# Optimization experiments

Measured on AMD Instinct MI355X. Metric: run time of the kernel, lower is better.

## Reference

```python
import jax, jax.numpy as jnp
import numpy as np
import math

S, HID = 2048, 2048
NH, Q_LORA, KV_LORA = 16, 1536, 512
NOPE, ROPE, VDIM = 128, 64, 128
HEAD = NOPE + ROPE  # 192
BLK = 128
EPS = 1e-6
MSCALE = 0.1 * 1.0 * math.log(40.0) + 1.0
SOFTMAX_SCALE = HEAD ** -0.5 * MSCALE * MSCALE


def _dequant(w, s, blk=BLK):
    # w: [out,in] stored quantized values, s: [ceil(out/blk), ceil(in/blk)] block scale_inv
    so = jnp.repeat(s, blk, axis=0)[: w.shape[0]]
    se = jnp.repeat(so, blk, axis=1)[:, : w.shape[1]]
    return w * se


def _mm_dq(x, w, s):
    # mm_w8a16_dq_forward: x @ dequant(w).T
    return x @ _dequant(w, s).T


def _rmsnorm(x, w, eps=EPS):
    var = jnp.mean(x * x, axis=-1, keepdims=True)
    return x * jax.lax.rsqrt(var + eps) * w


def _rotate_half(x):
    h = x.shape[-1] // 2
    return jnp.concatenate([-x[..., h:], x[..., :h]], axis=-1)


def setup_inputs() -> dict:
    key = jax.random.key(0)
    ks = jax.random.split(key, 16)
    d = {
        'hidden_states': jax.random.normal(ks[0], (S, HID), jnp.float32),
        'wq_a': jax.random.normal(ks[1], (Q_LORA, HID), jnp.float32),
        'sq_a': jax.random.uniform(ks[2], (12, 16), jnp.float32) * 0.02 + 0.005,
        'wq_b': jax.random.normal(ks[3], (NH * HEAD, Q_LORA), jnp.float32),
        'sq_b': jax.random.uniform(ks[4], (24, 12), jnp.float32) * 0.02 + 0.005,
        'wkv_a': jax.random.normal(ks[5], (KV_LORA + ROPE, HID), jnp.float32),
        'skv_a': jax.random.uniform(ks[6], (5, 16), jnp.float32) * 0.02 + 0.005,
        'wkv_b': jax.random.normal(ks[7], (NH * (NOPE + VDIM), KV_LORA), jnp.float32),
        'skv_b': jax.random.uniform(ks[8], (32, 4), jnp.float32) * 0.02 + 0.005,
        'wo': jax.random.normal(ks[9], (HID, NH * VDIM), jnp.float32),
        'so': jax.random.uniform(ks[10], (16, 16), jnp.float32) * 0.02 + 0.005,
        'q_ln_w': jnp.ones((Q_LORA,), jnp.float32),
        'kv_ln_w': jnp.ones((KV_LORA,), jnp.float32),
    }
    pos = jnp.arange(S, dtype=jnp.float32)[:, None]
    inv = 1.0 / (10000.0 ** (jnp.arange(0, ROPE, 2, dtype=jnp.float32) / ROPE))
    ang = pos * inv[None, :]
    ang = jnp.concatenate([ang, ang], axis=-1)  # [S, 64]
    d['cos'] = jnp.cos(ang)
    d['sin'] = jnp.sin(ang)
    return d


def reference(hidden_states, cos, sin, wq_a, sq_a, wq_b, sq_b, wkv_a, skv_a,
              wkv_b, skv_b, wo, so, q_ln_w, kv_ln_w):
    # Q low-rank path: q_a -> rmsnorm -> q_b
    lq = _mm_dq(hidden_states, wq_a, sq_a)                 # [S, q_lora]
    q = _mm_dq(_rmsnorm(lq, q_ln_w), wq_b, sq_b)           # [S, NH*HEAD]
    q = q.reshape(S, NH, HEAD)
    q_nope, q_pe = q[..., :NOPE], q[..., NOPE:]            # [S,NH,128], [S,NH,64]

    # KV low-rank + MQA rope path
    lkv = _mm_dq(hidden_states, wkv_a, skv_a)              # [S, kv_lora+rope]
    kv_nope = _rmsnorm(lkv[:, :KV_LORA], kv_ln_w)          # [S, kv_lora]
    k_pe = lkv[:, KV_LORA:]                                # [S, 64] (shared across heads)
    kvb = _mm_dq(kv_nope, wkv_b, skv_b).reshape(S, NH, NOPE + VDIM)
    k_nope, v = kvb[..., :NOPE], kvb[..., NOPE:]           # [S,NH,128] each

    # RoPE (rotate-half) on the pe parts
    q_pe = q_pe * cos[:, None, :] + _rotate_half(q_pe) * sin[:, None, :]
    k_pe = k_pe * cos + _rotate_half(k_pe) * sin           # [S, 64]

    # prefill MLA attention with causal mask
    scores = (jnp.einsum('shd,thd->hst', q_nope, k_nope)
              + jnp.einsum('shd,td->hst', q_pe, k_pe)) * SOFTMAX_SCALE
    causal = jnp.tril(jnp.ones((S, S), bool))
    scores = jnp.where(causal[None], scores, -jnp.inf)
    probs = jax.nn.softmax(scores, axis=-1)                # [NH,S,S]
    attn = jnp.einsum('hst,thd->shd', probs, v).reshape(S, NH * VDIM)

    return _mm_dq(attn, wo, so)                            # [S, HID]
```

## Files before the change

kernel.cpp:

```cpp
#include <hip/hip_runtime.h>

typedef unsigned short u16;
typedef unsigned int u32;
typedef __attribute__((ext_vector_type(8))) short bf16x8;
typedef __attribute__((ext_vector_type(4))) float f32x4;
typedef __attribute__((ext_vector_type(16))) float f32x16;
typedef __attribute__((ext_vector_type(4))) unsigned short u16x4;

#define S_LEN 2048
#define HIDDEN 2048
#define NHEAD 16
#define QLORA 1536
#define KVLORA 512
#define NOPE_D 128
#define ROPE_D 64
#define V_D 128
#define HEAD_D 192
#define NCOMB 2176
#define LOG2E 1.442695041f

__device__ __constant__ float SM_SCALE_C = (float)(0.07216878364870323 *
    ((0.1 * 3.6888794541139363 + 1.0) * (0.1 * 3.6888794541139363 + 1.0)));

__device__ inline u16 f2bf(float f) {
    union { float f; unsigned int u; } v; v.f = f;
    unsigned int r = v.u + 0x7FFFu + ((v.u >> 16) & 1u);
    return (u16)(r >> 16);
}
__device__ inline float bf2f(u16 b) {
    union { unsigned int u; float f; } v; v.u = ((unsigned int)b) << 16;
    return v.f;
}
__device__ inline void gload_lds16(const u16* g, u16* l) {
    __builtin_amdgcn_global_load_lds(
        (const __attribute__((address_space(1))) void*)g,
        (__attribute__((address_space(3))) void*)l, 16, 0, 0);
}

__global__ __launch_bounds__(64)
void prep_weights(const float* __restrict__ hs,
                  const float* __restrict__ wq_a, const float* __restrict__ sq_a,
                  const float* __restrict__ wq_b, const float* __restrict__ sq_b,
                  const float* __restrict__ wkv_a, const float* __restrict__ skv_a,
                  const float* __restrict__ wkv_b, const float* __restrict__ skv_b,
                  const float* __restrict__ wo, const float* __restrict__ so,
                  u16* __restrict__ hs_bf, u16* __restrict__ wcomb,
                  u16* __restrict__ wqb_bf, u16* __restrict__ wkvb_bf,
                  u16* __restrict__ wo_bf) {
    int r = blockIdx.x;
    const float* W; const float* Sc; u16* out; int K, sc_cols, n;
    if (r < 2048)                      { n = r;                     W = hs;    Sc = 0;     out = hs_bf;   K = 2048; sc_cols = 0; }
    else if (r < 2048 + 1536)          { n = r - 2048;              W = wq_a;  Sc = sq_a;  out = wcomb;   K = 2048; sc_cols = 16; }
    else if (r < 2048 + 1536 + 576)    { n = r - (2048 + 1536);     W = wkv_a; Sc = skv_a; out = wcomb + (size_t)QLORA * 2048; K = 2048; sc_cols = 16; }
    else if (r < 2048 + 1536 + 576 + 3072) { n = r - (2048 + 1536 + 576); W = wq_b; Sc = sq_b; out = wqb_bf; K = 1536; sc_cols = 12; }
    else if (r < 2048 + 1536 + 576 + 3072 + 4096) { n = r - (2048 + 1536 + 576 + 3072); W = wkv_b; Sc = skv_b; out = wkvb_bf; K = 512; sc_cols = 4; }
    else                               { n = r - (2048 + 1536 + 576 + 3072 + 4096); W = wo; Sc = so; out = wo_bf; K = 2048; sc_cols = 16; }
    for (int k = threadIdx.x * 8; k < K; k += 512) {
        float sc = Sc ? Sc[(n >> 7) * sc_cols + (k >> 7)] : 1.0f;
        f32x4 v0 = *(const f32x4*)(W + (size_t)n * K + k);
        f32x4 v1 = *(const f32x4*)(W + (size_t)n * K + k + 4);
        bf16x8 o;
        #pragma unroll
        for (int i = 0; i < 4; ++i) {
            o[i]     = (short)f2bf(v0[i] * sc);
            o[i + 4] = (short)f2bf(v1[i] * sc);
        }
        *(bf16x8*)(out + (size_t)n * K + k) = o;
    }
}

__global__ __launch_bounds__(256)
void gemm_bf16(const u16* __restrict__ A, const u16* __restrict__ W,
               void* __restrict__ C, int M, int N, int Ktot, int Ksub, int mode) {
    __shared__ u16 As[128 * 64];
    __shared__ u16 Ws[128 * 64];
    const int tid = threadIdx.x;
    const int lane = tid & 63;
    const int wv = tid >> 6;
    const int wm = wv >> 1, wn = wv & 1;
    const int gx = gridDim.x, gy = gridDim.y;
    const int nwg = gx * gy * gridDim.z;
    const int orig = blockIdx.x + gx * (blockIdx.y + gy * blockIdx.z);
    const int qq = nwg >> 3, rr = nwg & 7, xcd = orig & 7, loc = orig >> 3;
    const int wg = (xcd < rr) ? (xcd * (qq + 1) + loc)
                              : (rr * (qq + 1) + (xcd - rr) * qq + loc);
    const int bn = (wg % gx) * 128;
    const int bm = ((wg / gx) % gy) * 128;
    const int bz = wg / (gx * gy);
    const int lr = lane & 15, lk = lane >> 4;
    const int srow = lane >> 3;
    const int schunk = lane & 7;

    f32x4 acc[4][4] = {};

    const int kbeg = bz * Ksub;
    const int kend = kbeg + Ksub;
    for (int k0 = kbeg; k0 < kend; k0 += 64) {
        __syncthreads();
        #pragma unroll
        for (int i = 0; i < 4; ++i) {
            int t = (wv * 4 + i) * 8 + srow;
            int cs = (schunk ^ (t & 7)) << 3;
            gload_lds16(A + (size_t)(bm + t) * Ktot + k0 + cs, &As[(wv * 4 + i) * 512]);
            gload_lds16(W + (size_t)(bn + t) * Ktot + k0 + cs, &Ws[(wv * 4 + i) * 512]);
        }
        __syncthreads();
        #pragma unroll
        for (int kh = 0; kh < 2; ++kh) {
            bf16x8 af[4], bfr[4];
            #pragma unroll
            for (int mi = 0; mi < 4; ++mi) {
                int r = wm * 64 + mi * 16 + lr;
                af[mi] = *(const bf16x8*)&As[r * 64 + (((kh * 4 + lk) ^ (lr & 7)) << 3)];
            }
            #pragma unroll
            for (int ni = 0; ni < 4; ++ni) {
                int r = wn * 64 + ni * 16 + lr;
                bfr[ni] = *(const bf16x8*)&Ws[r * 64 + (((kh * 4 + lk) ^ (lr & 7)) << 3)];
            }
            #pragma unroll
            for (int mi = 0; mi < 4; ++mi)
                #pragma unroll
                for (int ni = 0; ni < 4; ++ni)
                    acc[mi][ni] = __builtin_amdgcn_mfma_f32_16x16x32_bf16(af[mi], bfr[ni], acc[mi][ni], 0, 0, 0);
        }
    }

    float* Pf = (mode == 2) ? ((float*)C + (size_t)bz * M * N) : (float*)C;
    #pragma unroll
    for (int mi = 0; mi < 4; ++mi)
        #pragma unroll
        for (int ni = 0; ni < 4; ++ni)
            #pragma unroll
            for (int j = 0; j < 4; ++j) {
                int r = bm + wm * 64 + mi * 16 + lk * 4 + j;
                int c = bn + wn * 64 + ni * 16 + lr;
                if (c < N) {
                    if (mode == 1) ((u16*)C)[(size_t)r * N + c] = f2bf(acc[mi][ni][j]);
                    else           Pf[(size_t)r * N + c] = acc[mi][ni][j];
                }
            }
}

__global__ __launch_bounds__(256)
void reduce_rms_comb(const float* __restrict__ P,
                     const float* __restrict__ q_ln, const float* __restrict__ kv_ln,
                     u16* __restrict__ lqn, u16* __restrict__ kvn, u16* __restrict__ kpe) {
    __shared__ float vbuf[NCOMB];
    __shared__ float r2[2][4];
    const int row = blockIdx.x;
    const float* p0 = P + (size_t)row * NCOMB;
    const float* p1 = p0 + (size_t)S_LEN * NCOMB;
    float ssq = 0.f, ssk = 0.f;
    for (int c = threadIdx.x * 4; c < NCOMB; c += 1024) {
        f32x4 a = *(const f32x4*)(p0 + c);
        f32x4 b = *(const f32x4*)(p1 + c);
        f32x4 v = a + b;
        *(f32x4*)&vbuf[c] = v;
        float s = v[0] * v[0] + v[1] * v[1] + v[2] * v[2] + v[3] * v[3];
        if (c < QLORA) ssq += s;
        else if (c < QLORA + KVLORA) ssk += s;
    }
    #pragma unroll
    for (int off = 1; off < 64; off <<= 1) {
        ssq += __shfl_xor(ssq, off, 64);
        ssk += __shfl_xor(ssk, off, 64);
    }
    if ((threadIdx.x & 63) == 0) {
        r2[0][threadIdx.x >> 6] = ssq;
        r2[1][threadIdx.x >> 6] = ssk;
    }
    __syncthreads();
    float rsq = rsqrtf((r2[0][0] + r2[0][1] + r2[0][2] + r2[0][3]) / (float)QLORA + 1e-6f);
    float rsk = rsqrtf((r2[1][0] + r2[1][1] + r2[1][2] + r2[1][3]) / (float)KVLORA + 1e-6f);
    for (int c = threadIdx.x * 4; c < NCOMB; c += 1024) {
        f32x4 v = *(const f32x4*)&vbuf[c];
        u16x4 o;
        if (c < QLORA) {
            #pragma unroll
            for (int j = 0; j < 4; ++j) o[j] = f2bf(v[j] * rsq * q_ln[c + j]);
            *(u16x4*)(lqn + (size_t)row * QLORA + c) = o;
        } else if (c < QLORA + KVLORA) {
            int cc = c - QLORA;
            #pragma unroll
            for (int j = 0; j < 4; ++j) o[j] = f2bf(v[j] * rsk * kv_ln[cc + j]);
            *(u16x4*)(kvn + (size_t)row * KVLORA + cc) = o;
        } else if (c < QLORA + KVLORA + ROPE_D) {
            int cc = c - QLORA - KVLORA;
            #pragma unroll
            for (int j = 0; j < 4; ++j) o[j] = f2bf(v[j]);
            *(u16x4*)(kpe + (size_t)row * ROPE_D + cc) = o;
        }
    }
}

__global__ __launch_bounds__(256)
void prep_q_frag_red(const float* __restrict__ P, const float* __restrict__ cosb,
                     const float* __restrict__ sinb, u16* __restrict__ qfrag) {
    const int sblk = blockIdx.x, h = blockIdx.y;
    const float sm = SM_SCALE_C;
    #pragma unroll
    for (int c = 0; c < 3; ++c) {
        int idx = c * 256 + threadIdx.x;
        int kk = idx >> 6;
        int lane = idx & 63;
        int s = sblk * 32 + (lane & 31);
        int d0 = kk * 16 + (lane >> 5) * 8;
        const float* p0 = P + (size_t)s * (NHEAD * HEAD_D) + h * HEAD_D;
        const float* p1 = p0 + (size_t)S_LEN * (NHEAD * HEAD_D);
        bf16x8 o;
        if (d0 < NOPE_D) {
            f32x4 a0 = *(const f32x4*)(p0 + d0), a1 = *(const f32x4*)(p0 + d0 + 4);
            f32x4 b0 = *(const f32x4*)(p1 + d0), b1 = *(const f32x4*)(p1 + d0 + 4);
            #pragma unroll
            for (int j = 0; j < 4; ++j) {
                o[j]     = (short)f2bf((a0[j] + b0[j]) * sm);
                o[j + 4] = (short)f2bf((a1[j] + b1[j]) * sm);
            }
        } else {
            int r0 = d0 - NOPE_D;
            int rp = (r0 + 32) & 63;
            float x[8], rv[8];
            {
                f32x4 a0 = *(const f32x4*)(p0 + d0), a1 = *(const f32x4*)(p0 + d0 + 4);
                f32x4 b0 = *(const f32x4*)(p1 + d0), b1 = *(const f32x4*)(p1 + d0 + 4);
                #pragma unroll
                for (int j = 0; j < 4; ++j) { x[j] = a0[j] + b0[j]; x[j + 4] = a1[j] + b1[j]; }
            }
            {
                f32x4 a0 = *(const f32x4*)(p0 + NOPE_D + rp), a1 = *(const f32x4*)(p0 + NOPE_D + rp + 4);
                f32x4 b0 = *(const f32x4*)(p1 + NOPE_D + rp), b1 = *(const f32x4*)(p1 + NOPE_D + rp + 4);
                #pragma unroll
                for (int j = 0; j < 4; ++j) { rv[j] = a0[j] + b0[j]; rv[j + 4] = a1[j] + b1[j]; }
            }
            float sign = (r0 < 32) ? -1.f : 1.f;
            #pragma unroll
            for (int j = 0; j < 8; ++j) {
                float cs = cosb[s * ROPE_D + r0 + j];
                float sn = sinb[s * ROPE_D + r0 + j];
                o[j] = (short)f2bf((x[j] * cs + sign * rv[j] * sn) * sm);
            }
        }
        *(bf16x8*)(qfrag + (((size_t)h * 64 + sblk) * 12 + kk) * 512 + lane * 8) = o;
    }
}

__global__ void reduce_out(const float* __restrict__ P, float* __restrict__ out, int n) {
    int i = (blockIdx.x * blockDim.x + threadIdx.x) * 4;
    if (i >= n) return;
    f32x4 a = *(const f32x4*)(P + i);
    f32x4 b = *(const f32x4*)(P + (size_t)n + i);
    *(f32x4*)(out + i) = a + b;
}

__global__ __launch_bounds__(256)
void prep_kv_frag(const u16* __restrict__ kvb, const u16* __restrict__ kpe,
                  const float* __restrict__ cosb, const float* __restrict__ sinb,
                  u16* __restrict__ kfrag, u16* __restrict__ vfrag) {
    __shared__ u16 Vs[32][136];
    const int sblk = blockIdx.x, h = blockIdx.y;
    #pragma unroll
    for (int it = 0; it < 2; ++it) {
        int idx = it * 256 + threadIdx.x;
        int r = idx >> 4;
        int c8 = (idx & 15) * 8;
        int s = sblk * 32 + r;
        *(bf16x8*)&Vs[r][c8] = *(const bf16x8*)(kvb + (size_t)s * (NHEAD * 256) + h * 256 + NOPE_D + c8);
    }
    #pragma unroll
    for (int c = 0; c < 3; ++c) {
        int idx = c * 256 + threadIdx.x;
        int kk = idx >> 6;
        int lane = idx & 63;
        int s = sblk * 32 + (lane & 31);
        int d0 = kk * 16 + (lane >> 5) * 8;
        bf16x8 o;
        if (d0 < NOPE_D) {
            o = *(const bf16x8*)(kvb + (size_t)s * (NHEAD * 256) + h * 256 + d0);
        } else {
            int r0 = d0 - NOPE_D;
            const u16* kp = kpe + (size_t)s * ROPE_D;
            bf16x8 x = *(const bf16x8*)(kp + r0);
            bf16x8 rv = *(const bf16x8*)(kp + ((r0 + 32) & 63));
            float sign = (r0 < 32) ? -1.f : 1.f;
            #pragma unroll
            for (int j = 0; j < 8; ++j) {
                float cs = cosb[s * ROPE_D + r0 + j];
                float sn = sinb[s * ROPE_D + r0 + j];
                o[j] = (short)f2bf(bf2f((u16)x[j]) * cs + sign * bf2f((u16)rv[j]) * sn);
            }
        }
        *(bf16x8*)(kfrag + (((size_t)h * 64 + sblk) * 12 + kk) * 512 + lane * 8) = o;
    }
    __syncthreads();
    #pragma unroll
    for (int it = 0; it < 2; ++it) {
        int idx = it * 256 + threadIdx.x;
        int fi = idx >> 6;
        int lane = idx & 63;
        int bb = fi >> 1, h16 = fi & 1;
        int col = bb * 32 + (lane & 31);
        int row0 = h16 * 16 + (lane >> 5) * 8;
        bf16x8 o;
        #pragma unroll
        for (int j = 0; j < 8; ++j) o[j] = (short)Vs[row0 + j][col];
        *(bf16x8*)(vfrag + (((size_t)h * 64 + sblk) * 8 + fi) * 512 + lane * 8) = o;
    }
}

__global__ __launch_bounds__(256, 2)
void flash_attn4(const u16* __restrict__ qfrag, const u16* __restrict__ kfrag,
                 const u16* __restrict__ vfrag, u16* __restrict__ attn) {
    __shared__ float OB[3][128][32];
    __shared__ float MB[3][2][32];

    const int tid = threadIdx.x, lane = tid & 63, wq = tid >> 6;
    const int b = blockIdx.x;
    const int t = 63 - (b >> 4);
    const int h = ((b & 7) << 1) | ((b >> 3) & 1);
    const int q0 = t * 32;
    const int lq = lane & 31;
    const int hi = lane >> 5;

    const int n = t + 1;
    const int s_lo = (wq * n) >> 2;
    const int s_hi = ((wq + 1) * n) >> 2;

    bf16x8 qfr[12];
    {
        const u16* qb = qfrag + (((size_t)h * 64 + t) * 12) * 512 + lane * 8;
        #pragma unroll
        for (int kk = 0; kk < 12; ++kk) qfr[kk] = *(const bf16x8*)(qb + kk * 512);
    }

    const u16* kfb = kfrag + ((size_t)h * 64 * 12) * 512 + lane * 8;
    const u16* vfb = vfrag + ((size_t)h * 64 * 8) * 512 + lane * 8;

    f32x16 oa[4] = {};
    float mrun = -3.0e38f, lrun = 0.f;

    bf16x8 kcur[12];
    {
        int psub = (s_lo < s_hi) ? s_lo : 0;
        const u16* kp = kfb + (size_t)psub * 12 * 512;
        #pragma unroll
        for (int kk = 0; kk < 12; ++kk)
            kcur[kk] = *(const bf16x8*)(kp + kk * 512);
    }

    for (int sub = s_lo; sub < s_hi; ++sub) {
        f32x16 s0 = {}, s1 = {};
        __builtin_amdgcn_s_setprio(1);
        #pragma unroll
        for (int kk = 0; kk < 12; kk += 2) {
            s0 = __builtin_amdgcn_mfma_f32_32x32x16_bf16(kcur[kk], qfr[kk], s0, 0, 0, 0);
            s1 = __builtin_amdgcn_mfma_f32_32x32x16_bf16(kcur[kk + 1], qfr[kk + 1], s1, 0, 0, 0);
        }
        __builtin_amdgcn_s_setprio(0);
        {
            int nsub = (sub + 1 < s_hi) ? sub + 1 : sub;
            const u16* kp = kfb + (size_t)nsub * 12 * 512;
            #pragma unroll
            for (int kk = 0; kk < 12; ++kk)
                kcur[kk] = *(const bf16x8*)(kp + kk * 512);
        }
        bf16x8 va[8];
        {
            const u16* vp = vfb + (size_t)sub * 8 * 512;
            #pragma unroll
            for (int fi = 0; fi < 8; ++fi)
                va[fi] = *(const bf16x8*)(vp + fi * 512);
        }
        f32x16 sv = s0 + s1;
        if (sub == t) {
            #pragma unroll
            for (int r = 0; r < 16; ++r) {
                int krow = (r & 3) + 8 * (r >> 2) + 4 * hi;
                if (krow > lq) sv[r] = -3.0e38f;
            }
        }
        float tm = sv[0];
        #pragma unroll
        for (int r = 1; r < 16; ++r) tm = fmaxf(tm, sv[r]);
        tm = fmaxf(tm, __shfl_xor(tm, 32, 64));
        if (!__all(tm - mrun <= 8.f)) {
            float mn = fmaxf(mrun, tm);
            float scl = exp2f((mrun - mn) * LOG2E);
            mrun = mn;
            lrun *= scl;
            #pragma unroll
            for (int bb = 0; bb < 4; ++bb)
                #pragma unroll
                for (int r = 0; r < 16; ++r) oa[bb][r] *= scl;
        }
        float p[16];
        float psum = 0.f;
        #pragma unroll
        for (int r = 0; r < 16; ++r) {
            p[r] = exp2f((sv[r] - mrun) * LOG2E);
            psum += p[r];
        }
        psum += __shfl_xor(psum, 32, 64);
        lrun += psum;
        u32 pw[8], sw[8];
        #pragma unroll
        for (int i = 0; i < 8; ++i)
            pw[i] = (u32)f2bf(p[2 * i]) | ((u32)f2bf(p[2 * i + 1]) << 16);
        #pragma unroll
        for (int i = 0; i < 8; ++i)
            sw[i] = (u32)__shfl_xor((int)pw[i], 32, 64);
        union { u32 w[4]; bf16x8 v; } bf0, bf1;
        bf0.w[0] = hi ? sw[2] : pw[0];
        bf0.w[1] = hi ? sw[3] : pw[1];
        bf0.w[2] = hi ? pw[2] : sw[0];
        bf0.w[3] = hi ? pw[3] : sw[1];
        bf1.w[0] = hi ? sw[6] : pw[4];
        bf1.w[1] = hi ? sw[7] : pw[5];
        bf1.w[2] = hi ? pw[6] : sw[4];
        bf1.w[3] = hi ? pw[7] : sw[5];
        __builtin_amdgcn_s_setprio(1);
        #pragma unroll
        for (int bb = 0; bb < 4; ++bb) {
            oa[bb] = __builtin_amdgcn_mfma_f32_32x32x16_bf16(va[bb * 2],     bf0.v, oa[bb], 0, 0, 0);
            oa[bb] = __builtin_amdgcn_mfma_f32_32x32x16_bf16(va[bb * 2 + 1], bf1.v, oa[bb], 0, 0, 0);
        }
        __builtin_amdgcn_s_setprio(0);
    }

    if (wq) {
        #pragma unroll
        for (int bb = 0; bb < 4; ++bb)
            #pragma unroll
            for (int r = 0; r < 16; ++r) {
                int dv = bb * 32 + (r & 3) + 8 * (r >> 2) + 4 * hi;
                OB[wq - 1][dv][lq] = oa[bb][r];
            }
        if (lane < 32) {
            MB[wq - 1][0][lane] = mrun;
            MB[wq - 1][1][lane] = lrun;
        }
    }
    __syncthreads();
    if (!wq) {
        float m1 = MB[0][0][lq], l1 = MB[0][1][lq];
        float m2 = MB[1][0][lq], l2 = MB[1][1][lq];
        float m3 = MB[2][0][lq], l3 = MB[2][1][lq];
        float M = fmaxf(fmaxf(mrun, m1), fmaxf(m2, m3));
        float e0 = exp2f((mrun - M) * LOG2E);
        float e1 = exp2f((m1 - M) * LOG2E);
        float e2 = exp2f((m2 - M) * LOG2E);
        float e3 = exp2f((m3 - M) * LOG2E);
        float L = lrun * e0 + l1 * e1 + l2 * e2 + l3 * e3;
        float inv = 1.0f / L;
        u16* ob = attn + (size_t)(q0 + lq) * (NHEAD * V_D) + h * V_D;
        #pragma unroll
        for (int bb = 0; bb < 4; ++bb)
            #pragma unroll
            for (int rq = 0; rq < 4; ++rq) {
                u16x4 pk;
                #pragma unroll
                for (int rb = 0; rb < 4; ++rb) {
                    int r = rq * 4 + rb;
                    int dv = bb * 32 + rb + 8 * rq + 4 * hi;
                    float o = (oa[bb][r] * e0 + OB[0][dv][lq] * e1 +
                               OB[1][dv][lq] * e2 + OB[2][dv][lq] * e3) * inv;
                    pk[rb] = f2bf(o);
                }
                *(u16x4*)(ob + bb * 32 + 8 * rq + 4 * hi) = pk;
            }
    }
}

extern "C" void kernel_launch(void* const* d_in, const int* in_sizes, int n_in,
                              void* d_out, int out_size, void* d_ws, size_t ws_size,
                              hipStream_t stream) {
    const float* hs    = (const float*)d_in[0];
    const float* wq_a  = (const float*)d_in[1];
    const float* sq_a  = (const float*)d_in[2];
    const float* wq_b  = (const float*)d_in[3];
    const float* sq_b  = (const float*)d_in[4];
    const float* wkv_a = (const float*)d_in[5];
    const float* skv_a = (const float*)d_in[6];
    const float* wkv_b = (const float*)d_in[7];
    const float* skv_b = (const float*)d_in[8];
    const float* wo    = (const float*)d_in[9];
    const float* so    = (const float*)d_in[10];
    const float* q_ln  = (const float*)d_in[11];
    const float* kv_ln = (const float*)d_in[12];
    const float* cosb  = (const float*)d_in[13];
    const float* sinb  = (const float*)d_in[14];
    float* out = (float*)d_out;

    char* ws = (char*)d_ws;
    size_t off = 0;
    auto alloc = [&](size_t bytes) -> void* {
        void* p = ws + off; off += (bytes + 255) & ~(size_t)255; return p;
    };
    u16* hs_bf  = (u16*)alloc((size_t)S_LEN * HIDDEN * 2);
    u16* lqn    = (u16*)alloc((size_t)S_LEN * QLORA * 2);
    u16* kvn    = (u16*)alloc((size_t)S_LEN * KVLORA * 2);
    u16* kpe    = (u16*)alloc((size_t)S_LEN * ROPE_D * 2);
    u16* kvb    = (u16*)alloc((size_t)S_LEN * NHEAD * 256 * 2);
    u16* attn   = (u16*)alloc((size_t)S_LEN * NHEAD * V_D * 2);
    u16* qfrag  = (u16*)alloc((size_t)NHEAD * 64 * 12 * 512 * 2);
    u16* kfrag  = (u16*)alloc((size_t)NHEAD * 64 * 12 * 512 * 2);
    u16* vfrag  = (u16*)alloc((size_t)NHEAD * 64 * 8 * 512 * 2);
    u16* wcomb  = (u16*)alloc((size_t)NCOMB * HIDDEN * 2);
    u16* wqb_bf  = (u16*)alloc((size_t)(NHEAD * HEAD_D) * QLORA * 2);
    u16* wkvb_bf = (u16*)alloc((size_t)(NHEAD * 256) * KVLORA * 2);
    u16* wo_bf   = (u16*)alloc((size_t)HIDDEN * (NHEAD * V_D) * 2);
    float* arena = (float*)alloc((size_t)2 * S_LEN * (NHEAD * HEAD_D) * 4);

    prep_weights<<<2048 + 1536 + 576 + 3072 + 4096 + 2048, 64, 0, stream>>>(
        hs, wq_a, sq_a, wq_b, sq_b, wkv_a, skv_a, wkv_b, skv_b, wo, so,
        hs_bf, wcomb, wqb_bf, wkvb_bf, wo_bf);

    gemm_bf16<<<dim3(NCOMB / 128, S_LEN / 128, 2), 256, 0, stream>>>(hs_bf, wcomb, arena,
        S_LEN, NCOMB, HIDDEN, HIDDEN / 2, 2);
    reduce_rms_comb<<<S_LEN, 256, 0, stream>>>(arena, q_ln, kv_ln, lqn, kvn, kpe);

    gemm_bf16<<<dim3(NHEAD * HEAD_D / 128, S_LEN / 128, 2), 256, 0, stream>>>(lqn, wqb_bf, arena,
        S_LEN, NHEAD * HEAD_D, QLORA, QLORA / 2, 2);
    prep_q_frag_red<<<dim3(64, NHEAD), 256, 0, stream>>>(arena, cosb, sinb, qfrag);

    gemm_bf16<<<dim3(NHEAD * 256 / 128, S_LEN / 128, 1), 256, 0, stream>>>(kvn, wkvb_bf, kvb,
        S_LEN, NHEAD * 256, KVLORA, KVLORA, 1);

    prep_kv_frag<<<dim3(64, NHEAD), 256, 0, stream>>>(kvb, kpe, cosb, sinb, kfrag, vfrag);

    flash_attn4<<<1024, 256, 0, stream>>>(qfrag, kfrag, vfrag, attn);

    gemm_bf16<<<dim3(HIDDEN / 128, S_LEN / 128, 2), 256, 0, stream>>>(attn, wo_bf, arena,
        S_LEN, HIDDEN, NHEAD * V_D, (NHEAD * V_D) / 2, 2);
    reduce_out<<<(S_LEN * HIDDEN / 4 + 255) / 256, 256, 0, stream>>>(arena, out, S_LEN * HIDDEN);
}
```

Baseline: 232.0 us.

## Raise split-K factors and merge q_b and kv_b GEMMs into one launch

The hidden-state and output-projection GEMMs now split K four ways instead of two, and the q_b GEMM splits K three ways. The q_b GEMM and the independent kv_b GEMM are combined into a single grid that dispatches by workgroup index. The reduction kernels (reduce_rms_comb, prep_q_frag_red, reduce_out) are updated to sum the extra partials, and the fp32 scratch arena is enlarged to hold them. The aim is to fill all CUs on these fairly small-grid GEMMs and to remove one launch and its tail. The cost is more fp32 partial-sum traffic written and re-read by the reductions.

```diff
diff --git a/kernel.cpp b/kernel.cpp
--- a/kernel.cpp
+++ b/kernel.cpp
@@ -69,24 +69,14 @@
     }
 }
 
-__global__ __launch_bounds__(256)
-void gemm_bf16(const u16* __restrict__ A, const u16* __restrict__ W,
-               void* __restrict__ C, int M, int N, int Ktot, int Ksub, int mode) {
-    __shared__ u16 As[128 * 64];
-    __shared__ u16 Ws[128 * 64];
+__device__ __forceinline__ void gemm_core(
+    const u16* __restrict__ A, const u16* __restrict__ W, void* __restrict__ C,
+    int M, int N, int Ktot, int Ksub, int mode, int bm, int bn, int bz,
+    u16* As, u16* Ws) {
     const int tid = threadIdx.x;
     const int lane = tid & 63;
     const int wv = tid >> 6;
     const int wm = wv >> 1, wn = wv & 1;
-    const int gx = gridDim.x, gy = gridDim.y;
-    const int nwg = gx * gy * gridDim.z;
-    const int orig = blockIdx.x + gx * (blockIdx.y + gy * blockIdx.z);
-    const int qq = nwg >> 3, rr = nwg & 7, xcd = orig & 7, loc = orig >> 3;
-    const int wg = (xcd < rr) ? (xcd * (qq + 1) + loc)
-                              : (rr * (qq + 1) + (xcd - rr) * qq + loc);
-    const int bn = (wg % gx) * 128;
-    const int bm = ((wg / gx) % gy) * 128;
-    const int bz = wg / (gx * gy);
     const int lr = lane & 15, lk = lane >> 4;
     const int srow = lane >> 3;
     const int schunk = lane & 7;
@@ -140,6 +130,47 @@
                     else           Pf[(size_t)r * N + c] = acc[mi][ni][j];
                 }
             }
+}
+
+__device__ __forceinline__ int xcd_swizzle(int orig, int nwg) {
+    int qq = nwg >> 3, rr = nwg & 7, xcd = orig & 7, loc = orig >> 3;
+    return (xcd < rr) ? (xcd * (qq + 1) + loc)
+                      : (rr * (qq + 1) + (xcd - rr) * qq + loc);
+}
+
+__global__ __launch_bounds__(256)
+void gemm_bf16(const u16* __restrict__ A, const u16* __restrict__ W,
+               void* __restrict__ C, int M, int N, int Ktot, int Ksub, int mode) {
+    __shared__ u16 As[128 * 64];
+    __shared__ u16 Ws[128 * 64];
+    const int gx = gridDim.x, gy = gridDim.y;
+    const int nwg = gx * gy * gridDim.z;
+    const int orig = blockIdx.x + gx * (blockIdx.y + gy * blockIdx.z);
+    const int wg = xcd_swizzle(orig, nwg);
+    const int bn = (wg % gx) * 128;
+    const int bm = ((wg / gx) % gy) * 128;
+    const int bz = wg / (gx * gy);
+    gemm_core(A, W, C, M, N, Ktot, Ksub, mode, bm, bn, bz, As, Ws);
+}
+
+__global__ __launch_bounds__(256)
+void gemm_qh_kvb(const u16* __restrict__ lqn, const u16* __restrict__ wqb, float* __restrict__ arena,
+                 const u16* __restrict__ kvn, const u16* __restrict__ wkvb, u16* __restrict__ kvb) {
+    __shared__ u16 As[128 * 64];
+    __shared__ u16 Ws[128 * 64];
+    const int NWG = 24 * 16 * 3 + 32 * 16;
+    const int wg = xcd_swizzle(blockIdx.x, NWG);
+    if (wg < 24 * 16 * 3) {
+        const int bn = (wg % 24) * 128;
+        const int bm = ((wg / 24) % 16) * 128;
+        const int bz = wg / (24 * 16);
+        gemm_core(lqn, wqb, arena, S_LEN, NHEAD * HEAD_D, QLORA, 512, 2, bm, bn, bz, As, Ws);
+    } else {
+        const int w2 = wg - 24 * 16 * 3;
+        const int bn = (w2 % 32) * 128;
+        const int bm = (w2 / 32) * 128;
+        gemm_core(kvn, wkvb, kvb, S_LEN, NHEAD * 256, KVLORA, 512, 1, bm, bn, 0, As, Ws);
+    }
 }
 
 __global__ __launch_bounds__(256)
@@ -150,12 +181,13 @@
     __shared__ float r2[2][4];
     const int row = blockIdx.x;
     const float* p0 = P + (size_t)row * NCOMB;
-    const float* p1 = p0 + (size_t)S_LEN * NCOMB;
+    const size_t st = (size_t)S_LEN * NCOMB;
     float ssq = 0.f, ssk = 0.f;
     for (int c = threadIdx.x * 4; c < NCOMB; c += 1024) {
-        f32x4 a = *(const f32x4*)(p0 + c);
-        f32x4 b = *(const f32x4*)(p1 + c);
-        f32x4 v = a + b;
+        f32x4 v = *(const f32x4*)(p0 + c);
+        v += *(const f32x4*)(p0 + st + c);
+        v += *(const f32x4*)(p0 + 2 * st + c);
+        v += *(const f32x4*)(p0 + 3 * st + c);
         *(f32x4*)&vbuf[c] = v;
         float s = v[0] * v[0] + v[1] * v[1] + v[2] * v[2] + v[3] * v[3];
         if (c < QLORA) ssq += s;
@@ -199,6 +231,7 @@
                      const float* __restrict__ sinb, u16* __restrict__ qfrag) {
     const int sblk = blockIdx.x, h = blockIdx.y;
     const float sm = SM_SCALE_C;
+    const size_t st = (size_t)S_LEN * (NHEAD * HEAD_D);
     #pragma unroll
     for (int c = 0; c < 3; ++c) {
         int idx = c * 256 + threadIdx.x;
@@ -207,32 +240,25 @@
         int s = sblk * 32 + (lane & 31);
         int d0 = kk * 16 + (lane >> 5) * 8;
         const float* p0 = P + (size_t)s * (NHEAD * HEAD_D) + h * HEAD_D;
-        const float* p1 = p0 + (size_t)S_LEN * (NHEAD * HEAD_D);
         bf16x8 o;
         if (d0 < NOPE_D) {
-            f32x4 a0 = *(const f32x4*)(p0 + d0), a1 = *(const f32x4*)(p0 + d0 + 4);
-            f32x4 b0 = *(const f32x4*)(p1 + d0), b1 = *(const f32x4*)(p1 + d0 + 4);
+            f32x4 a0 = *(const f32x4*)(p0 + d0) + *(const f32x4*)(p0 + st + d0) + *(const f32x4*)(p0 + 2 * st + d0);
+            f32x4 a1 = *(const f32x4*)(p0 + d0 + 4) + *(const f32x4*)(p0 + st + d0 + 4) + *(const f32x4*)(p0 + 2 * st + d0 + 4);
             #pragma unroll
             for (int j = 0; j < 4; ++j) {
-                o[j]     = (short)f2bf((a0[j] + b0[j]) * sm);
-                o[j + 4] = (short)f2bf((a1[j] + b1[j]) * sm);
+                o[j]     = (short)f2bf(a0[j] * sm);
+                o[j + 4] = (short)f2bf(a1[j] * sm);
             }
         } else {
             int r0 = d0 - NOPE_D;
             int rp = (r0 + 32) & 63;
+            f32x4 x0 = *(const f32x4*)(p0 + d0) + *(const f32x4*)(p0 + st + d0) + *(const f32x4*)(p0 + 2 * st + d0);
+            f32x4 x1 = *(const f32x4*)(p0 + d0 + 4) + *(const f32x4*)(p0 + st + d0 + 4) + *(const f32x4*)(p0 + 2 * st + d0 + 4);
+            f32x4 r0v = *(const f32x4*)(p0 + NOPE_D + rp) + *(const f32x4*)(p0 + st + NOPE_D + rp) + *(const f32x4*)(p0 + 2 * st + NOPE_D + rp);
+            f32x4 r1v = *(const f32x4*)(p0 + NOPE_D + rp + 4) + *(const f32x4*)(p0 + st + NOPE_D + rp + 4) + *(const f32x4*)(p0 + 2 * st + NOPE_D + rp + 4);
             float x[8], rv[8];
-            {
-                f32x4 a0 = *(const f32x4*)(p0 + d0), a1 = *(const f32x4*)(p0 + d0 + 4);
-                f32x4 b0 = *(const f32x4*)(p1 + d0), b1 = *(const f32x4*)(p1 + d0 + 4);
-                #pragma unroll
-                for (int j = 0; j < 4; ++j) { x[j] = a0[j] + b0[j]; x[j + 4] = a1[j] + b1[j]; }
-            }
-            {
-                f32x4 a0 = *(const f32x4*)(p0 + NOPE_D + rp), a1 = *(const f32x4*)(p0 + NOPE_D + rp + 4);
-                f32x4 b0 = *(const f32x4*)(p1 + NOPE_D + rp), b1 = *(const f32x4*)(p1 + NOPE_D + rp + 4);
-                #pragma unroll
-                for (int j = 0; j < 4; ++j) { rv[j] = a0[j] + b0[j]; rv[j + 4] = a1[j] + b1[j]; }
-            }
+            #pragma unroll
+            for (int j = 0; j < 4; ++j) { x[j] = x0[j]; x[j + 4] = x1[j]; rv[j] = r0v[j]; rv[j + 4] = r1v[j]; }
             float sign = (r0 < 32) ? -1.f : 1.f;
             #pragma unroll
             for (int j = 0; j < 8; ++j) {
@@ -248,9 +274,11 @@
 __global__ void reduce_out(const float* __restrict__ P, float* __restrict__ out, int n) {
     int i = (blockIdx.x * blockDim.x + threadIdx.x) * 4;
     if (i >= n) return;
-    f32x4 a = *(const f32x4*)(P + i);
-    f32x4 b = *(const f32x4*)(P + (size_t)n + i);
-    *(f32x4*)(out + i) = a + b;
+    f32x4 v = *(const f32x4*)(P + i);
+    v += *(const f32x4*)(P + (size_t)n + i);
+    v += *(const f32x4*)(P + 2 * (size_t)n + i);
+    v += *(const f32x4*)(P + 3 * (size_t)n + i);
+    *(f32x4*)(out + i) = v;
 }
 
 __global__ __launch_bounds__(256)
@@ -509,28 +537,24 @@
     u16* wqb_bf  = (u16*)alloc((size_t)(NHEAD * HEAD_D) * QLORA * 2);
     u16* wkvb_bf = (u16*)alloc((size_t)(NHEAD * 256) * KVLORA * 2);
     u16* wo_bf   = (u16*)alloc((size_t)HIDDEN * (NHEAD * V_D) * 2);
-    float* arena = (float*)alloc((size_t)2 * S_LEN * (NHEAD * HEAD_D) * 4);
+    float* arena = (float*)alloc((size_t)3 * S_LEN * (NHEAD * HEAD_D) * 4);
 
     prep_weights<<<2048 + 1536 + 576 + 3072 + 4096 + 2048, 64, 0, stream>>>(
         hs, wq_a, sq_a, wq_b, sq_b, wkv_a, skv_a, wkv_b, skv_b, wo, so,
         hs_bf, wcomb, wqb_bf, wkvb_bf, wo_bf);
 
-    gemm_bf16<<<dim3(NCOMB / 128, S_LEN / 128, 2), 256, 0, stream>>>(hs_bf, wcomb, arena,
-        S_LEN, NCOMB, HIDDEN, HIDDEN / 2, 2);
+    gemm_bf16<<<dim3(NCOMB / 128, S_LEN / 128, 4), 256, 0, stream>>>(hs_bf, wcomb, arena,
+        S_LEN, NCOMB, HIDDEN, HIDDEN / 4, 2);
     reduce_rms_comb<<<S_LEN, 256, 0, stream>>>(arena, q_ln, kv_ln, lqn, kvn, kpe);
 
-    gemm_bf16<<<dim3(NHEAD * HEAD_D / 128, S_LEN / 128, 2), 256, 0, stream>>>(lqn, wqb_bf, arena,
-        S_LEN, NHEAD * HEAD_D, QLORA, QLORA / 2, 2);
+    gemm_qh_kvb<<<24 * 16 * 3 + 32 * 16, 256, 0, stream>>>(lqn, wqb_bf, arena, kvn, wkvb_bf, kvb);
     prep_q_frag_red<<<dim3(64, NHEAD), 256, 0, stream>>>(arena, cosb, sinb, qfrag);
 
-    gemm_bf16<<<dim3(NHEAD * 256 / 128, S_LEN / 128, 1), 256, 0, stream>>>(kvn, wkvb_bf, kvb,
-        S_LEN, NHEAD * 256, KVLORA, KVLORA, 1);
-
     prep_kv_frag<<<dim3(64, NHEAD), 256, 0, stream>>>(kvb, kpe, cosb, sinb, kfrag, vfrag);
 
     flash_attn4<<<1024, 256, 0, stream>>>(qfrag, kfrag, vfrag, attn);
 
-    gemm_bf16<<<dim3(HIDDEN / 128, S_LEN / 128, 2), 256, 0, stream>>>(attn, wo_bf, arena,
-        S_LEN, HIDDEN, NHEAD * V_D, (NHEAD * V_D) / 2, 2);
+    gemm_bf16<<<dim3(HIDDEN / 128, S_LEN / 128, 4), 256, 0, stream>>>(attn, wo_bf, arena,
+        S_LEN, HIDDEN, NHEAD * V_D, (NHEAD * V_D) / 4, 2);
     reduce_out<<<(S_LEN * HIDDEN / 4 + 255) / 256, 256, 0, stream>>>(arena, out, S_LEN * HIDDEN);
 }
```

After: 239.8 us. +3.4%, slower.
